# Kernel tuning notes

Hardware: AMD Instinct MI355X
Metric: run time of the kernel (lower is better)

## Reference

```python
import jax, jax.numpy as jnp
import numpy as np

B, T_TRG, T_SRC, C, H = 2, 2048, 2048, 512, 8
HD = C // H

def setup_inputs() -> dict:
    key = jax.random.key(0)
    ks = jax.random.split(key, 10)
    s = 0.02
    return {
        'x': jax.random.normal(ks[0], (B, T_TRG, C), jnp.float32),
        'encoder_outputs': jax.random.normal(ks[1], (B, T_SRC, C), jnp.float32),
        'padding_mask': jnp.ones((B, T_SRC), jnp.int32),
        'Wq': jax.random.normal(ks[2], (C, C), jnp.float32) * s,
        'bq': jnp.zeros((C,), jnp.float32),
        'Wk': jax.random.normal(ks[3], (C, C), jnp.float32) * s,
        'bk': jnp.zeros((C,), jnp.float32),
        'Wv': jax.random.normal(ks[4], (C, C), jnp.float32) * s,
        'bv': jnp.zeros((C,), jnp.float32),
        'Wo': jax.random.normal(ks[5], (C, C), jnp.float32) * s,
        'bo': jnp.zeros((C,), jnp.float32),
    }

def reference(x, encoder_outputs, padding_mask, Wq, bq, Wk, bk, Wv, bv, Wo, bo):
    Bx, Tt, Cx = x.shape
    Ts = encoder_outputs.shape[1]
    scale = HD ** -0.5
    # projections (nn.Linear: y = x @ W.T + b; here W stored as [in,out])
    q = (x @ Wq + bq).reshape(Bx, Tt, H, HD).transpose(0, 2, 1, 3)            # [B,H,Tt,HD]
    k = (encoder_outputs @ Wk + bk).reshape(Bx, Ts, H, HD).transpose(0, 2, 1, 3)
    v = (encoder_outputs @ Wv + bv).reshape(Bx, Ts, H, HD).transpose(0, 2, 1, 3)
    scores = jnp.einsum('bhqd,bhkd->bhqk', q, k) * scale                      # [B,H,Tt,Ts]
    mask = padding_mask[:, None, None, :] != 0                                # [B,1,1,Ts]
    scores = jnp.where(mask, scores, jnp.float32(-jnp.inf))
    probs = jax.nn.softmax(scores, axis=-1)
    # dropout: identity at inference
    out = jnp.einsum('bhqk,bhkd->bhqd', probs, v)                             # [B,H,Tt,HD]
    out = out.transpose(0, 2, 1, 3).reshape(Bx, Tt, Cx)
    return out @ Wo + bo
```

## Files before the change

kernel.cpp:

```cpp
#include <hip/hip_runtime.h>

#define TT 2048
#define TS 2048
#define NB 2
#define CC 512
#define NH 8
#define HD 64
#define NCH 2
#define KCH (TS / NCH)
#define NROW (NB * NH * TT)

typedef __attribute__((ext_vector_type(8))) short s8v;
typedef __attribute__((ext_vector_type(8))) __bf16 bf8v;
typedef __attribute__((ext_vector_type(4))) float f4v;
typedef __attribute__((ext_vector_type(4))) unsigned short us4;

static __device__ __forceinline__ unsigned short f2bf(float f) {
  unsigned int u = __builtin_bit_cast(unsigned int, f);
  u += 0x7FFFu + ((u >> 16) & 1u);
  return (unsigned short)(u >> 16);
}
static __device__ __forceinline__ float bf2f(unsigned short u) {
  return __builtin_bit_cast(float, (unsigned int)u << 16);
}
static __device__ __forceinline__ bf8v ld_bf8(const unsigned short* p) {
  return __builtin_bit_cast(bf8v, *(const s8v*)p);
}
static __device__ __forceinline__ f4v mfma16(bf8v a, bf8v b, f4v c) {
  return __builtin_amdgcn_mfma_f32_16x16x32_bf16(a, b, c, 0, 0, 0);
}
static __device__ __forceinline__ void gll16(const unsigned short* g,
                                             unsigned short* l) {
  __builtin_amdgcn_global_load_lds(
      (const __attribute__((address_space(1))) unsigned int*)g,
      (__attribute__((address_space(3))) unsigned int*)l, 16, 0, 0);
}

__global__ __launch_bounds__(256) void prep_k(const float* __restrict__ W0,
    const float* __restrict__ W1, const float* __restrict__ W2, const float* __restrict__ W3,
    unsigned short* __restrict__ T0, unsigned short* __restrict__ T1,
    unsigned short* __restrict__ T2, unsigned short* __restrict__ T3,
    const float* __restrict__ x, const float* __restrict__ enc,
    const int* __restrict__ mask, unsigned short* __restrict__ xb,
    unsigned short* __restrict__ eb, float* __restrict__ pinf) {
  __shared__ float t[64][65];
  int id = blockIdx.x;
  if (id < 256) {
    const float* Ws[4] = {W0, W1, W2, W3};
    unsigned short* Ts[4] = {T0, T1, T2, T3};
    const float* W = Ws[id >> 6];
    unsigned short* WT = Ts[id >> 6];
    int blk = id & 63;
    int i0 = (blk >> 3) * 64, j0 = (blk & 7) * 64;
    int tx = threadIdx.x & 63, ty = threadIdx.x >> 6;
#pragma unroll
    for (int r = 0; r < 16; r++) {
      int li = ty * 16 + r;
      t[li][tx] = W[(size_t)(i0 + li) * CC + j0 + tx];
    }
    __syncthreads();
#pragma unroll
    for (int r = 0; r < 16; r++) {
      int lj = ty * 16 + r;
      WT[(size_t)(j0 + lj) * CC + i0 + tx] = f2bf(t[tx][lj]);
    }
  } else {
    size_t tt = (size_t)(id - 256) * 256 + threadIdx.x;
    size_t i = tt * 4;
    f4v a = *(const f4v*)(x + i);
    f4v b = *(const f4v*)(enc + i);
    us4 pa, pb;
#pragma unroll
    for (int j = 0; j < 4; j++) { pa[j] = f2bf(a[j]); pb[j] = f2bf(b[j]); }
    *(us4*)(xb + i) = pa;
    *(us4*)(eb + i) = pb;
    if (tt < NB * TS) pinf[tt] = (mask[tt] != 0) ? 0.0f : -1e30f;
  }
}

__global__ __launch_bounds__(256) void qkv_k(
    const unsigned short* __restrict__ xb, const unsigned short* __restrict__ eb,
    const unsigned short* __restrict__ WqT, const unsigned short* __restrict__ WkT,
    const unsigned short* __restrict__ WvT,
    const float* __restrict__ bq, const float* __restrict__ bk,
    const float* __restrict__ bv,
    unsigned short* __restrict__ Qb, unsigned short* __restrict__ Kb,
    unsigned short* __restrict__ VTb) {
  __shared__ unsigned short Al[2][128 * 64];
  __shared__ unsigned short Bl[2][64 * 64];
  int op = blockIdx.z;
  const unsigned short* A = (op == 0) ? xb : eb;
  const unsigned short* W = (op == 0) ? WqT : (op == 1 ? WkT : WvT);
  const float* bias = (op == 0) ? bq : (op == 1 ? bk : bv);
  int lane = threadIdx.x & 63, wave = threadIdx.x >> 6;
  int quad = lane >> 4, l16 = lane & 15;
  int r8 = lane >> 3, g8 = (lane & 7) ^ r8;
  int m0 = blockIdx.x * 128, n0 = blockIdx.y * 64;
  const unsigned short* Ag = A + (size_t)m0 * CC + g8 * 8;
  const unsigned short* Wg = W + (size_t)n0 * CC + g8 * 8;
  f4v acc[2][4];
#pragma unroll
  for (int s = 0; s < 2; s++)
#pragma unroll
    for (int n = 0; n < 4; n++) acc[s][n] = (f4v){0, 0, 0, 0};
#pragma unroll
  for (int j = 0; j < 4; j++)
    gll16(Ag + (size_t)(wave * 32 + j * 8 + r8) * CC, &Al[0][(wave * 32 + j * 8) * 64]);
#pragma unroll
  for (int j = 0; j < 2; j++)
    gll16(Wg + (size_t)(wave * 16 + j * 8 + r8) * CC, &Bl[0][(wave * 16 + j * 8) * 64]);
  int buf = 0;
  for (int k0 = 0; k0 < CC; k0 += 64) {
    __syncthreads();
    int sw = (quad ^ (l16 & 7)) * 8;
    bf8v af[2][2], bfr[4][2];
#pragma unroll
    for (int sub = 0; sub < 2; sub++)
#pragma unroll
      for (int kk = 0; kk < 2; kk++)
        af[sub][kk] = ld_bf8(&Al[buf][(wave * 32 + sub * 16 + l16) * 64 + (sw ^ (kk * 32))]);
#pragma unroll
    for (int nt = 0; nt < 4; nt++)
#pragma unroll
      for (int kk = 0; kk < 2; kk++)
        bfr[nt][kk] = ld_bf8(&Bl[buf][(nt * 16 + l16) * 64 + (sw ^ (kk * 32))]);
    if (k0 + 64 < CC) {
#pragma unroll
      for (int j = 0; j < 4; j++)
        gll16(Ag + (size_t)(wave * 32 + j * 8 + r8) * CC + k0 + 64,
              &Al[buf ^ 1][(wave * 32 + j * 8) * 64]);
#pragma unroll
      for (int j = 0; j < 2; j++)
        gll16(Wg + (size_t)(wave * 16 + j * 8 + r8) * CC + k0 + 64,
              &Bl[buf ^ 1][(wave * 16 + j * 8) * 64]);
    }
#pragma unroll
    for (int kk = 0; kk < 2; kk++)
#pragma unroll
      for (int sub = 0; sub < 2; sub++)
#pragma unroll
        for (int nt = 0; nt < 4; nt++)
          acc[sub][nt] = mfma16(af[sub][kk], bfr[nt][kk], acc[sub][nt]);
    buf ^= 1;
  }
  const float QSC = 0.125f * 1.44269504088896340736f;
#pragma unroll
  for (int sub = 0; sub < 2; sub++) {
    int row0 = m0 + wave * 32 + sub * 16 + quad * 4;
#pragma unroll
    for (int nt = 0; nt < 4; nt++) {
      int col = n0 + nt * 16 + l16;
      float bcol = bias[col];
      if (op == 2) {
        int bb = row0 >> 11, tt = row0 & (TT - 1);
        us4 pk;
#pragma unroll
        for (int r = 0; r < 4; r++) pk[r] = f2bf(acc[sub][nt][r] + bcol);
        *(us4*)(VTb + ((size_t)bb * CC + col) * TS + tt) = pk;
      } else {
        unsigned short* O = (op == 0) ? Qb : Kb;
        float sc = (op == 0) ? QSC : 1.0f;
#pragma unroll
        for (int r = 0; r < 4; r++)
          O[(size_t)(row0 + r) * CC + col] = f2bf((acc[sub][nt][r] + bcol) * sc);
      }
    }
  }
}

__global__ __launch_bounds__(256) void attn_k(const unsigned short* __restrict__ Q,
    const unsigned short* __restrict__ K, const unsigned short* __restrict__ VT,
    const float* __restrict__ pinf, unsigned short* __restrict__ Op,
    float* __restrict__ Lp) {
  __shared__ unsigned short Kl[2][64 * 64];
  __shared__ unsigned short Vl[2][64 * 64];
  __shared__ unsigned short Pl[4][2][16 * 72];
  int lane = threadIdx.x & 63, wave = threadIdx.x >> 6;
  int quad = lane >> 4, l16 = lane & 15;
  int r8 = lane >> 3, g8 = (lane & 7) ^ r8;
  int id = blockIdx.x;
  int bh = id & 15, qblk = (id >> 4) & 15, chunk = id >> 8;
  int b = bh >> 3, h = bh & 7;
  int q0 = qblk * 128 + wave * 32;
  int ck0 = chunk * KCH;

  bf8v qa[2][2];
#pragma unroll
  for (int sub = 0; sub < 2; sub++) {
    const unsigned short* qp =
        Q + (size_t)(b * TT + q0 + sub * 16 + l16) * CC + h * HD + quad * 8;
    qa[sub][0] = ld_bf8(qp);
    qa[sub][1] = ld_bf8(qp + 32);
  }

  f4v o[2][4];
#pragma unroll
  for (int s = 0; s < 2; s++)
#pragma unroll
    for (int d = 0; d < 4; d++) o[s][d] = (f4v){0, 0, 0, 0};
  f4v ls[2] = {{0, 0, 0, 0}, {0, 0, 0, 0}};
  const float* prow = pinf + (size_t)b * TS + ck0;
  const unsigned short* Kg = K + (size_t)(b * TS + ck0) * CC + h * HD + g8 * 8;
  const unsigned short* Vg = VT + ((size_t)b * CC + h * HD) * TS + ck0 + g8 * 8;

#pragma unroll
  for (int j = 0; j < 2; j++) {
    int row = wave * 16 + j * 8;
    gll16(Kg + (size_t)(row + r8) * CC, &Kl[0][row * 64]);
    gll16(Vg + (size_t)(row + r8) * TS, &Vl[0][row * 64]);
  }
  int buf = 0;
  for (int kt = 0; kt < KCH; kt += 64) {
    __syncthreads();
    int sw = (quad ^ (l16 & 7)) * 8;
    bf8v kf[4][2], vf[4][2];
    f4v pen[4];
#pragma unroll
    for (int nt = 0; nt < 4; nt++) {
      kf[nt][0] = ld_bf8(&Kl[buf][(nt * 16 + l16) * 64 + sw]);
      kf[nt][1] = ld_bf8(&Kl[buf][(nt * 16 + l16) * 64 + (sw ^ 32)]);
      vf[nt][0] = ld_bf8(&Vl[buf][(nt * 16 + l16) * 64 + sw]);
      vf[nt][1] = ld_bf8(&Vl[buf][(nt * 16 + l16) * 64 + (sw ^ 32)]);
      pen[nt] = *(const f4v*)(prow + kt + nt * 16 + quad * 4);
    }
    if (kt + 64 < KCH) {
#pragma unroll
      for (int j = 0; j < 2; j++) {
        int row = wave * 16 + j * 8;
        gll16(Kg + (size_t)(kt + 64 + row + r8) * CC, &Kl[buf ^ 1][row * 64]);
        gll16(Vg + (size_t)(row + r8) * TS + kt + 64, &Vl[buf ^ 1][row * 64]);
      }
    }
#pragma unroll
    for (int sub = 0; sub < 2; sub++) {
      f4v s[4];
#pragma unroll
      for (int nt = 0; nt < 4; nt++) {
        f4v z = pen[nt];
        z = mfma16(kf[nt][0], qa[sub][0], z);
        z = mfma16(kf[nt][1], qa[sub][1], z);
        s[nt] = z;
      }
      unsigned short* pw = &Pl[wave][sub][0];
#pragma unroll
      for (int nt = 0; nt < 4; nt++) {
        us4 pk;
#pragma unroll
        for (int r = 0; r < 4; r++) {
          float p = __builtin_amdgcn_exp2f(s[nt][r]);
          s[nt][r] = p;
          pk[r] = f2bf(p);
        }
        ls[sub] += s[nt];
        *(us4*)&pw[l16 * 72 + nt * 16 + quad * 4] = pk;
      }
      bf8v pb0 = ld_bf8(&pw[l16 * 72 + quad * 8]);
      bf8v pb1 = ld_bf8(&pw[l16 * 72 + 32 + quad * 8]);
#pragma unroll
      for (int dt = 0; dt < 4; dt++) {
        o[sub][dt] = mfma16(vf[dt][0], pb0, o[sub][dt]);
        o[sub][dt] = mfma16(vf[dt][1], pb1, o[sub][dt]);
      }
    }
    buf ^= 1;
  }
#pragma unroll
  for (int sub = 0; sub < 2; sub++) {
    float l = (ls[sub][0] + ls[sub][1]) + (ls[sub][2] + ls[sub][3]);
    l += __shfl_xor(l, 16, 64);
    l += __shfl_xor(l, 32, 64);
    int rowb = (b * NH + h) * TT + q0 + sub * 16;
    size_t obase = (size_t)chunk * NROW * HD + (size_t)(rowb + l16) * HD;
#pragma unroll
    for (int dt = 0; dt < 4; dt++) {
      us4 pk;
#pragma unroll
      for (int r = 0; r < 4; r++) pk[r] = f2bf(o[sub][dt][r]);
      *(us4*)&Op[obase + dt * 16 + quad * 4] = pk;
    }
    if (quad == 0) Lp[(size_t)chunk * NROW + rowb + l16] = l;
  }
}

__global__ __launch_bounds__(256) void gemmo_k(const unsigned short* __restrict__ Op,
    const float* __restrict__ Lp, const unsigned short* __restrict__ WoT,
    const float* __restrict__ bo, float* __restrict__ outf) {
  __shared__ unsigned short Al[2][128 * 64];
  __shared__ unsigned short Bl[2][64 * 64];
  int lane = threadIdx.x & 63, wave = threadIdx.x >> 6;
  int quad = lane >> 4, l16 = lane & 15;
  int r8 = lane >> 3, lc = lane & 7, g8 = lc ^ r8;
  int m0 = blockIdx.x * 128, n0 = blockIdx.y * 64;
  const unsigned short* Wg = WoT + (size_t)n0 * CC + g8 * 8;
  f4v acc[2][4];
#pragma unroll
  for (int s = 0; s < 2; s++)
#pragma unroll
    for (int n = 0; n < 4; n++) acc[s][n] = (f4v){0, 0, 0, 0};

  auto stage_a = [&](int k0, int dbuf) {
    int h = k0 >> 6;
#pragma unroll
    for (int j = 0; j < 4; j++) {
      int rr = wave * 32 + j * 8 + r8;
      int m = m0 + rr;
      int bb = m >> 11, q = m & (TT - 1);
      size_t rowb = (size_t)((bb * NH + h) * TT + q);
      int gd = (lc ^ r8) * 8;
      s8v o0 = *(const s8v*)(Op + rowb * HD + gd);
      s8v o1 = *(const s8v*)(Op + (size_t)NROW * HD + rowb * HD + gd);
      float L = Lp[rowb] + Lp[NROW + rowb];
      float inv = __builtin_amdgcn_rcpf(L);
      s8v pk;
#pragma unroll
      for (int e = 0; e < 8; e++) {
        float v = (bf2f((unsigned short)o0[e]) + bf2f((unsigned short)o1[e])) * inv;
        pk[e] = (short)f2bf(v);
      }
      *(s8v*)&Al[dbuf][rr * 64 + lc * 8] = pk;
    }
  };

  stage_a(0, 0);
#pragma unroll
  for (int j = 0; j < 2; j++)
    gll16(Wg + (size_t)(wave * 16 + j * 8 + r8) * CC, &Bl[0][(wave * 16 + j * 8) * 64]);
  int buf = 0;
  for (int k0 = 0; k0 < CC; k0 += 64) {
    __syncthreads();
    int sw = (quad ^ (l16 & 7)) * 8;
    bf8v af[2][2], bfr[4][2];
#pragma unroll
    for (int sub = 0; sub < 2; sub++)
#pragma unroll
      for (int kk = 0; kk < 2; kk++)
        af[sub][kk] = ld_bf8(&Al[buf][(wave * 32 + sub * 16 + l16) * 64 + (sw ^ (kk * 32))]);
#pragma unroll
    for (int nt = 0; nt < 4; nt++)
#pragma unroll
      for (int kk = 0; kk < 2; kk++)
        bfr[nt][kk] = ld_bf8(&Bl[buf][(nt * 16 + l16) * 64 + (sw ^ (kk * 32))]);
    if (k0 + 64 < CC) {
      stage_a(k0 + 64, buf ^ 1);
#pragma unroll
      for (int j = 0; j < 2; j++)
        gll16(Wg + (size_t)(wave * 16 + j * 8 + r8) * CC + k0 + 64,
              &Bl[buf ^ 1][(wave * 16 + j * 8) * 64]);
    }
#pragma unroll
    for (int kk = 0; kk < 2; kk++)
#pragma unroll
      for (int sub = 0; sub < 2; sub++)
#pragma unroll
        for (int nt = 0; nt < 4; nt++)
          acc[sub][nt] = mfma16(af[sub][kk], bfr[nt][kk], acc[sub][nt]);
    buf ^= 1;
  }
#pragma unroll
  for (int sub = 0; sub < 2; sub++) {
    int row0 = m0 + wave * 32 + sub * 16 + quad * 4;
#pragma unroll
    for (int nt = 0; nt < 4; nt++) {
      int col = n0 + nt * 16 + l16;
      float bcol = bo[col];
#pragma unroll
      for (int r = 0; r < 4; r++)
        outf[(size_t)(row0 + r) * CC + col] = acc[sub][nt][r] + bcol;
    }
  }
}

extern "C" void kernel_launch(void* const* d_in, const int* in_sizes, int n_in,
                              void* d_out, int out_size, void* d_ws, size_t ws_size,
                              hipStream_t stream) {
  const float* x   = (const float*)d_in[0];
  const float* enc = (const float*)d_in[1];
  const int*   msk = (const int*)d_in[2];
  const float* Wq  = (const float*)d_in[3];
  const float* bq  = (const float*)d_in[4];
  const float* Wk  = (const float*)d_in[5];
  const float* bk  = (const float*)d_in[6];
  const float* Wv  = (const float*)d_in[7];
  const float* bv  = (const float*)d_in[8];
  const float* Wo  = (const float*)d_in[9];
  const float* bo  = (const float*)d_in[10];
  float* out = (float*)d_out;

  char* ws = (char*)d_ws;
  const size_t MB = 1024 * 1024;
  unsigned short* WqT  = (unsigned short*)(ws);
  unsigned short* WkT  = (unsigned short*)(ws + 512 * 1024);
  unsigned short* WvT  = (unsigned short*)(ws + 1024 * 1024);
  unsigned short* WoT  = (unsigned short*)(ws + 1536 * 1024);
  unsigned short* Qb   = (unsigned short*)(ws + 2 * MB);
  unsigned short* Kb   = (unsigned short*)(ws + 6 * MB);
  unsigned short* VTb  = (unsigned short*)(ws + 10 * MB);
  unsigned short* xb   = (unsigned short*)(ws + 18 * MB);
  unsigned short* eb   = (unsigned short*)(ws + 22 * MB);
  unsigned short* Opart = (unsigned short*)(ws + 18 * MB);
  float* Lp   = (float*)(ws + 34 * MB);
  float* pinf = (float*)(ws + 35 * MB);

  dim3 blk(256);
  prep_k<<<dim3(2304), blk, 0, stream>>>(Wq, Wk, Wv, Wo, WqT, WkT, WvT, WoT,
                                         x, enc, msk, xb, eb, pinf);

  qkv_k<<<dim3(32, 8, 3), blk, 0, stream>>>(xb, eb, WqT, WkT, WvT,
                                            bq, bk, bv, Qb, Kb, VTb);

  attn_k<<<dim3(512), blk, 0, stream>>>(Qb, Kb, VTb, pinf, Opart, Lp);

  gemmo_k<<<dim3(32, 8), blk, 0, stream>>>(Opart, Lp, WoT, bo, out);
}
```

Before: 146.5 us.

## Split attention over four key chunks and halve GEMM row tiles for parallelism

Raises the attention split-K chunk count from two to four, doubling the attention grid, and makes the output GEMM combine four partial results. Halves the M tile of the QKV and output-projection GEMMs from 128 to 64 rows, doubling their grid sizes. The mask is now converted to a penalty inside the attention loop instead of in a separate pinf buffer written by the prep kernel. The aim is to fill more of the GPU's compute units per launch. The cost is more partial-output traffic, a four-way reduction in the output GEMM, and less data reuse per GEMM block.

Result: slower. 152.9 us (+4.4%).

```diff
diff --git a/kernel.cpp b/kernel.cpp
--- a/kernel.cpp
+++ b/kernel.cpp
@@ -6,13 +6,14 @@
 #define CC 512
 #define NH 8
 #define HD 64
-#define NCH 2
+#define NCH 4
 #define KCH (TS / NCH)
 #define NROW (NB * NH * TT)
 
 typedef __attribute__((ext_vector_type(8))) short s8v;
 typedef __attribute__((ext_vector_type(8))) __bf16 bf8v;
 typedef __attribute__((ext_vector_type(4))) float f4v;
+typedef __attribute__((ext_vector_type(4))) int i4v;
 typedef __attribute__((ext_vector_type(4))) unsigned short us4;
 
 static __device__ __forceinline__ unsigned short f2bf(float f) {
@@ -41,8 +42,7 @@
     unsigned short* __restrict__ T0, unsigned short* __restrict__ T1,
     unsigned short* __restrict__ T2, unsigned short* __restrict__ T3,
     const float* __restrict__ x, const float* __restrict__ enc,
-    const int* __restrict__ mask, unsigned short* __restrict__ xb,
-    unsigned short* __restrict__ eb, float* __restrict__ pinf) {
+    unsigned short* __restrict__ xb, unsigned short* __restrict__ eb) {
   __shared__ float t[64][65];
   int id = blockIdx.x;
   if (id < 256) {
@@ -74,7 +74,6 @@
     for (int j = 0; j < 4; j++) { pa[j] = f2bf(a[j]); pb[j] = f2bf(b[j]); }
     *(us4*)(xb + i) = pa;
     *(us4*)(eb + i) = pb;
-    if (tt < NB * TS) pinf[tt] = (mask[tt] != 0) ? 0.0f : -1e30f;
   }
 }
 
@@ -86,7 +85,7 @@
     const float* __restrict__ bv,
     unsigned short* __restrict__ Qb, unsigned short* __restrict__ Kb,
     unsigned short* __restrict__ VTb) {
-  __shared__ unsigned short Al[2][128 * 64];
+  __shared__ unsigned short Al[2][64 * 64];
   __shared__ unsigned short Bl[2][64 * 64];
   int op = blockIdx.z;
   const unsigned short* A = (op == 0) ? xb : eb;
@@ -95,30 +94,26 @@
   int lane = threadIdx.x & 63, wave = threadIdx.x >> 6;
   int quad = lane >> 4, l16 = lane & 15;
   int r8 = lane >> 3, g8 = (lane & 7) ^ r8;
-  int m0 = blockIdx.x * 128, n0 = blockIdx.y * 64;
+  int m0 = blockIdx.x * 64, n0 = blockIdx.y * 64;
   const unsigned short* Ag = A + (size_t)m0 * CC + g8 * 8;
   const unsigned short* Wg = W + (size_t)n0 * CC + g8 * 8;
-  f4v acc[2][4];
-#pragma unroll
-  for (int s = 0; s < 2; s++)
-#pragma unroll
-    for (int n = 0; n < 4; n++) acc[s][n] = (f4v){0, 0, 0, 0};
-#pragma unroll
-  for (int j = 0; j < 4; j++)
-    gll16(Ag + (size_t)(wave * 32 + j * 8 + r8) * CC, &Al[0][(wave * 32 + j * 8) * 64]);
-#pragma unroll
-  for (int j = 0; j < 2; j++)
-    gll16(Wg + (size_t)(wave * 16 + j * 8 + r8) * CC, &Bl[0][(wave * 16 + j * 8) * 64]);
+  f4v acc[4];
+#pragma unroll
+  for (int n = 0; n < 4; n++) acc[n] = (f4v){0, 0, 0, 0};
+#pragma unroll
+  for (int j = 0; j < 2; j++) {
+    int row = wave * 16 + j * 8;
+    gll16(Ag + (size_t)(row + r8) * CC, &Al[0][row * 64]);
+    gll16(Wg + (size_t)(row + r8) * CC, &Bl[0][row * 64]);
+  }
   int buf = 0;
   for (int k0 = 0; k0 < CC; k0 += 64) {
     __syncthreads();
     int sw = (quad ^ (l16 & 7)) * 8;
-    bf8v af[2][2], bfr[4][2];
-#pragma unroll
-    for (int sub = 0; sub < 2; sub++)
-#pragma unroll
-      for (int kk = 0; kk < 2; kk++)
-        af[sub][kk] = ld_bf8(&Al[buf][(wave * 32 + sub * 16 + l16) * 64 + (sw ^ (kk * 32))]);
+    bf8v af[2], bfr[4][2];
+#pragma unroll
+    for (int kk = 0; kk < 2; kk++)
+      af[kk] = ld_bf8(&Al[buf][(wave * 16 + l16) * 64 + (sw ^ (kk * 32))]);
 #pragma unroll
     for (int nt = 0; nt < 4; nt++)
 #pragma unroll
@@ -126,51 +121,44 @@
         bfr[nt][kk] = ld_bf8(&Bl[buf][(nt * 16 + l16) * 64 + (sw ^ (kk * 32))]);
     if (k0 + 64 < CC) {
 #pragma unroll
-      for (int j = 0; j < 4; j++)
-        gll16(Ag + (size_t)(wave * 32 + j * 8 + r8) * CC + k0 + 64,
-              &Al[buf ^ 1][(wave * 32 + j * 8) * 64]);
-#pragma unroll
-      for (int j = 0; j < 2; j++)
-        gll16(Wg + (size_t)(wave * 16 + j * 8 + r8) * CC + k0 + 64,
-              &Bl[buf ^ 1][(wave * 16 + j * 8) * 64]);
+      for (int j = 0; j < 2; j++) {
+        int row = wave * 16 + j * 8;
+        gll16(Ag + (size_t)(row + r8) * CC + k0 + 64, &Al[buf ^ 1][row * 64]);
+        gll16(Wg + (size_t)(row + r8) * CC + k0 + 64, &Bl[buf ^ 1][row * 64]);
+      }
     }
 #pragma unroll
     for (int kk = 0; kk < 2; kk++)
 #pragma unroll
-      for (int sub = 0; sub < 2; sub++)
-#pragma unroll
-        for (int nt = 0; nt < 4; nt++)
-          acc[sub][nt] = mfma16(af[sub][kk], bfr[nt][kk], acc[sub][nt]);
+      for (int nt = 0; nt < 4; nt++)
+        acc[nt] = mfma16(af[kk], bfr[nt][kk], acc[nt]);
     buf ^= 1;
   }
   const float QSC = 0.125f * 1.44269504088896340736f;
-#pragma unroll
-  for (int sub = 0; sub < 2; sub++) {
-    int row0 = m0 + wave * 32 + sub * 16 + quad * 4;
-#pragma unroll
-    for (int nt = 0; nt < 4; nt++) {
-      int col = n0 + nt * 16 + l16;
-      float bcol = bias[col];
-      if (op == 2) {
-        int bb = row0 >> 11, tt = row0 & (TT - 1);
-        us4 pk;
-#pragma unroll
-        for (int r = 0; r < 4; r++) pk[r] = f2bf(acc[sub][nt][r] + bcol);
-        *(us4*)(VTb + ((size_t)bb * CC + col) * TS + tt) = pk;
-      } else {
-        unsigned short* O = (op == 0) ? Qb : Kb;
-        float sc = (op == 0) ? QSC : 1.0f;
-#pragma unroll
-        for (int r = 0; r < 4; r++)
-          O[(size_t)(row0 + r) * CC + col] = f2bf((acc[sub][nt][r] + bcol) * sc);
-      }
+  int row0 = m0 + wave * 16 + quad * 4;
+#pragma unroll
+  for (int nt = 0; nt < 4; nt++) {
+    int col = n0 + nt * 16 + l16;
+    float bcol = bias[col];
+    if (op == 2) {
+      int bb = row0 >> 11, tt = row0 & (TT - 1);
+      us4 pk;
+#pragma unroll
+      for (int r = 0; r < 4; r++) pk[r] = f2bf(acc[nt][r] + bcol);
+      *(us4*)(VTb + ((size_t)bb * CC + col) * TS + tt) = pk;
+    } else {
+      unsigned short* O = (op == 0) ? Qb : Kb;
+      float sc = (op == 0) ? QSC : 1.0f;
+#pragma unroll
+      for (int r = 0; r < 4; r++)
+        O[(size_t)(row0 + r) * CC + col] = f2bf((acc[nt][r] + bcol) * sc);
     }
   }
 }
 
 __global__ __launch_bounds__(256) void attn_k(const unsigned short* __restrict__ Q,
     const unsigned short* __restrict__ K, const unsigned short* __restrict__ VT,
-    const float* __restrict__ pinf, unsigned short* __restrict__ Op,
+    const int* __restrict__ mask, unsigned short* __restrict__ Op,
     float* __restrict__ Lp) {
   __shared__ unsigned short Kl[2][64 * 64];
   __shared__ unsigned short Vl[2][64 * 64];
@@ -199,7 +187,7 @@
 #pragma unroll
     for (int d = 0; d < 4; d++) o[s][d] = (f4v){0, 0, 0, 0};
   f4v ls[2] = {{0, 0, 0, 0}, {0, 0, 0, 0}};
-  const float* prow = pinf + (size_t)b * TS + ck0;
+  const int* mrow = mask + (size_t)b * TS + ck0;
   const unsigned short* Kg = K + (size_t)(b * TS + ck0) * CC + h * HD + g8 * 8;
   const unsigned short* Vg = VT + ((size_t)b * CC + h * HD) * TS + ck0 + g8 * 8;
 
@@ -221,7 +209,9 @@
       kf[nt][1] = ld_bf8(&Kl[buf][(nt * 16 + l16) * 64 + (sw ^ 32)]);
       vf[nt][0] = ld_bf8(&Vl[buf][(nt * 16 + l16) * 64 + sw]);
       vf[nt][1] = ld_bf8(&Vl[buf][(nt * 16 + l16) * 64 + (sw ^ 32)]);
-      pen[nt] = *(const f4v*)(prow + kt + nt * 16 + quad * 4);
+      i4v mk = *(const i4v*)(mrow + kt + nt * 16 + quad * 4);
+#pragma unroll
+      for (int r = 0; r < 4; r++) pen[nt][r] = (mk[r] != 0) ? 0.0f : -1e30f;
     }
     if (kt + 64 < KCH) {
 #pragma unroll
@@ -285,37 +275,41 @@
 __global__ __launch_bounds__(256) void gemmo_k(const unsigned short* __restrict__ Op,
     const float* __restrict__ Lp, const unsigned short* __restrict__ WoT,
     const float* __restrict__ bo, float* __restrict__ outf) {
-  __shared__ unsigned short Al[2][128 * 64];
+  __shared__ unsigned short Al[2][64 * 64];
   __shared__ unsigned short Bl[2][64 * 64];
   int lane = threadIdx.x & 63, wave = threadIdx.x >> 6;
   int quad = lane >> 4, l16 = lane & 15;
   int r8 = lane >> 3, lc = lane & 7, g8 = lc ^ r8;
-  int m0 = blockIdx.x * 128, n0 = blockIdx.y * 64;
+  int m0 = blockIdx.x * 64, n0 = blockIdx.y * 64;
   const unsigned short* Wg = WoT + (size_t)n0 * CC + g8 * 8;
-  f4v acc[2][4];
-#pragma unroll
-  for (int s = 0; s < 2; s++)
-#pragma unroll
-    for (int n = 0; n < 4; n++) acc[s][n] = (f4v){0, 0, 0, 0};
+  f4v acc[4];
+#pragma unroll
+  for (int n = 0; n < 4; n++) acc[n] = (f4v){0, 0, 0, 0};
 
   auto stage_a = [&](int k0, int dbuf) {
     int h = k0 >> 6;
 #pragma unroll
-    for (int j = 0; j < 4; j++) {
-      int rr = wave * 32 + j * 8 + r8;
+    for (int j = 0; j < 2; j++) {
+      int rr = wave * 16 + j * 8 + r8;
       int m = m0 + rr;
       int bb = m >> 11, q = m & (TT - 1);
       size_t rowb = (size_t)((bb * NH + h) * TT + q);
       int gd = (lc ^ r8) * 8;
-      s8v o0 = *(const s8v*)(Op + rowb * HD + gd);
-      s8v o1 = *(const s8v*)(Op + (size_t)NROW * HD + rowb * HD + gd);
-      float L = Lp[rowb] + Lp[NROW + rowb];
+      s8v oc[NCH];
+      float L = 0.f;
+#pragma unroll
+      for (int c = 0; c < NCH; c++) {
+        oc[c] = *(const s8v*)(Op + (size_t)c * NROW * HD + rowb * HD + gd);
+        L += Lp[(size_t)c * NROW + rowb];
+      }
       float inv = __builtin_amdgcn_rcpf(L);
       s8v pk;
 #pragma unroll
       for (int e = 0; e < 8; e++) {
-        float v = (bf2f((unsigned short)o0[e]) + bf2f((unsigned short)o1[e])) * inv;
-        pk[e] = (short)f2bf(v);
+        float v = 0.f;
+#pragma unroll
+        for (int c = 0; c < NCH; c++) v += bf2f((unsigned short)oc[c][e]);
+        pk[e] = (short)f2bf(v * inv);
       }
       *(s8v*)&Al[dbuf][rr * 64 + lc * 8] = pk;
     }
@@ -329,12 +323,10 @@
   for (int k0 = 0; k0 < CC; k0 += 64) {
     __syncthreads();
     int sw = (quad ^ (l16 & 7)) * 8;
-    bf8v af[2][2], bfr[4][2];
-#pragma unroll
-    for (int sub = 0; sub < 2; sub++)
-#pragma unroll
-      for (int kk = 0; kk < 2; kk++)
-        af[sub][kk] = ld_bf8(&Al[buf][(wave * 32 + sub * 16 + l16) * 64 + (sw ^ (kk * 32))]);
+    bf8v af[2], bfr[4][2];
+#pragma unroll
+    for (int kk = 0; kk < 2; kk++)
+      af[kk] = ld_bf8(&Al[buf][(wave * 16 + l16) * 64 + (sw ^ (kk * 32))]);
 #pragma unroll
     for (int nt = 0; nt < 4; nt++)
 #pragma unroll
@@ -350,23 +342,18 @@
 #pragma unroll
     for (int kk = 0; kk < 2; kk++)
 #pragma unroll
-      for (int sub = 0; sub < 2; sub++)
-#pragma unroll
-        for (int nt = 0; nt < 4; nt++)
-          acc[sub][nt] = mfma16(af[sub][kk], bfr[nt][kk], acc[sub][nt]);
+      for (int nt = 0; nt < 4; nt++)
+        acc[nt] = mfma16(af[kk], bfr[nt][kk], acc[nt]);
     buf ^= 1;
   }
-#pragma unroll
-  for (int sub = 0; sub < 2; sub++) {
-    int row0 = m0 + wave * 32 + sub * 16 + quad * 4;
-#pragma unroll
-    for (int nt = 0; nt < 4; nt++) {
-      int col = n0 + nt * 16 + l16;
-      float bcol = bo[col];
-#pragma unroll
-      for (int r = 0; r < 4; r++)
-        outf[(size_t)(row0 + r) * CC + col] = acc[sub][nt][r] + bcol;
-    }
+  int row0 = m0 + wave * 16 + quad * 4;
+#pragma unroll
+  for (int nt = 0; nt < 4; nt++) {
+    int col = n0 + nt * 16 + l16;
+    float bcol = bo[col];
+#pragma unroll
+    for (int r = 0; r < 4; r++)
+      outf[(size_t)(row0 + r) * CC + col] = acc[nt][r] + bcol;
   }
 }
 
@@ -399,16 +386,15 @@
   unsigned short* eb   = (unsigned short*)(ws + 22 * MB);
   unsigned short* Opart = (unsigned short*)(ws + 18 * MB);
   float* Lp   = (float*)(ws + 34 * MB);
-  float* pinf = (float*)(ws + 35 * MB);
 
   dim3 blk(256);
   prep_k<<<dim3(2304), blk, 0, stream>>>(Wq, Wk, Wv, Wo, WqT, WkT, WvT, WoT,
-                                         x, enc, msk, xb, eb, pinf);
-
-  qkv_k<<<dim3(32, 8, 3), blk, 0, stream>>>(xb, eb, WqT, WkT, WvT,
+                                         x, enc, xb, eb);
+
+  qkv_k<<<dim3(64, 8, 3), blk, 0, stream>>>(xb, eb, WqT, WkT, WvT,
                                             bq, bk, bv, Qb, Kb, VTb);
 
-  attn_k<<<dim3(512), blk, 0, stream>>>(Qb, Kb, VTb, pinf, Opart, Lp);
-
-  gemmo_k<<<dim3(32, 8), blk, 0, stream>>>(Opart, Lp, WoT, bo, out);
-}
+  attn_k<<<dim3(1024), blk, 0, stream>>>(Qb, Kb, VTb, msk, Opart, Lp);
+
+  gemmo_k<<<dim3(64, 8), blk, 0, stream>>>(Opart, Lp, WoT, bo, out);
+}
```
